# Kernel optimization log

Measured on AMD Instinct MI355X. Metric: run time of the kernel, lower is better.

The kernel has to match this reference:

```python
import jax, jax.numpy as jnp
import numpy as np

TEMP = 0.07
EPS = 1e-8
THRESH = 0.0          # self.global_threshold default
NORM_EPS = 1e-12      # F.normalize default eps


def setup_inputs() -> dict:
    key = jax.random.key(0)
    k1, k2, k3 = jax.random.split(key, 3)
    T, C, H, W = 8, 256, 64, 64
    return {
        "current_preds": jax.random.uniform(k1, (T, 1, H, W), jnp.float32),
        "history_preds": jax.random.uniform(k2, (T, 1, H, W), jnp.float32),
        "features": jax.random.normal(k3, (T, C, H, W), jnp.float32),
        "epoch": 1,
    }


def _supervised_labels(current_preds, history_preds):
    # Deviation per video (Dice-like metrics on binarized preds), then select
    # current pred if dev <= threshold else history pred (both detached).
    T = current_preds.shape[0]
    cb = (current_preds > 0.5).astype(jnp.float32).reshape(T, -1)
    hb = (history_preds > 0.5).astype(jnp.float32).reshape(T, -1)
    e1 = (cb * hb).sum(axis=1)
    e2 = cb.sum(axis=1) + hb.sum(axis=1)
    m1 = (2.0 * e1 + EPS) / (e2 + EPS)
    m2 = (e1 + EPS) / (e2 - e1 + EPS)
    dev = 1.0 - (m1 + m2) / 2.0                       # [T]
    use_curr = (dev <= THRESH)[:, None, None, None]
    return jnp.where(use_curr, current_preds, history_preds)


def _contrastive_loss(features, labels):
    T, C, H, W = features.shape
    N = H * W
    feat = features.reshape(T, C, N).transpose(0, 2, 1)            # [T,N,C]
    nrm = jnp.linalg.norm(feat, axis=-1, keepdims=True)
    feat = feat / jnp.maximum(nrm, NORM_EPS)                       # L2 normalize
    lbl = labels.reshape(T, N)
    fg = lbl > 0.5
    bg = ~fg
    sim = jnp.einsum('tnc,tmc->tnm', feat, feat) / TEMP            # [T,N,N]
    pos = jnp.exp(jnp.diagonal(sim, axis1=1, axis2=2))             # [T,N]
    # neg_i = sum over bg columns of exp(sim); masked matvec honors fg/bg split
    neg = jnp.einsum('tnm,tm->tn', jnp.exp(sim), bg.astype(feat.dtype))
    per_pix = -jnp.log(pos / (pos + neg + EPS))                    # [T,N]
    fgf = fg.astype(feat.dtype)
    n_fg = fgf.sum(axis=1)
    frame_loss = (per_pix * fgf).sum(axis=1) / jnp.maximum(n_fg, 1.0)  # mean over fg
    valid = (fg.any(axis=1) & bg.any(axis=1)).astype(feat.dtype)   # frames with both
    n_valid = valid.sum()
    return jnp.where(n_valid > 0,
                     (frame_loss * valid).sum() / jnp.maximum(n_valid, 1.0),
                     jnp.zeros((), feat.dtype))


def reference(current_preds, history_preds, features, epoch):
    # epoch >= 1 path of DOC.forward (epoch==0 only populates memory)
    labels = jax.lax.stop_gradient(_supervised_labels(current_preds, history_preds))
    loss = _contrastive_loss(features, labels)
    return (labels, loss)
```

## Files before the change

### kernel.cpp

```cpp
#include <hip/hip_runtime.h>
#include <hip/hip_bf16.h>
#include <cstdint>
#include <cstddef>

constexpr int T = 8;
constexpr int C = 256;
constexpr int N = 4096;
constexpr float TEMP_INV = 14.285714285714286f;
constexpr float EPS = 1e-8f;

typedef __bf16 bf16;
typedef __bf16 bf16x8 __attribute__((ext_vector_type(8)));
typedef float floatx4 __attribute__((ext_vector_type(4)));

__device__ __forceinline__ void async_copy16(const bf16* g, bf16* l) {
    __builtin_amdgcn_global_load_lds((const __attribute__((address_space(1))) void*)g,
                                     (__attribute__((address_space(3))) void*)l,
                                     16, 0, 0);
}

__global__ void stats_kernel(const float* __restrict__ cur,
                             const float* __restrict__ hist,
                             float* __restrict__ flag,
                             int* __restrict__ nfg, int* __restrict__ nbg) {
    int t = blockIdx.x;
    int tid = threadIdx.x;
    float s1 = 0.f, sc = 0.f, sh = 0.f;
    for (int k = tid; k < N; k += 256) {
        float c = cur[t * N + k] > 0.5f ? 1.f : 0.f;
        float h = hist[t * N + k] > 0.5f ? 1.f : 0.f;
        s1 += c * h; sc += c; sh += h;
    }
    for (int o = 32; o > 0; o >>= 1) {
        s1 += __shfl_down(s1, o);
        sc += __shfl_down(sc, o);
        sh += __shfl_down(sh, o);
    }
    __shared__ float r1[4], r2[4], r3[4];
    int w = tid >> 6;
    if ((tid & 63) == 0) { r1[w] = s1; r2[w] = sc; r3[w] = sh; }
    __syncthreads();
    if (tid == 0) {
        float e1 = r1[0] + r1[1] + r1[2] + r1[3];
        float scs = r2[0] + r2[1] + r2[2] + r2[3];
        float shs = r3[0] + r3[1] + r3[2] + r3[3];
        float e2 = scs + shs;
        float m1 = (2.f * e1 + EPS) / (e2 + EPS);
        float m2 = (e1 + EPS) / (e2 - e1 + EPS);
        float dev = 1.f - 0.5f * (m1 + m2);
        flag[t] = (dev <= 0.0f) ? 1.f : 0.f;
        nfg[t] = 0;
        nbg[t] = 0;
    }
}

__global__ void labels_kernel(const float* __restrict__ cur,
                              const float* __restrict__ hist,
                              const float* __restrict__ flag,
                              float* __restrict__ out_labels,
                              float* __restrict__ negbuf,
                              unsigned short* __restrict__ fgidx,
                              unsigned short* __restrict__ bgidx,
                              int* __restrict__ nfg, int* __restrict__ nbg) {
    int t = blockIdx.x;
    int tid = threadIdx.x;
    int lane = tid & 63;
    bool use_curr = flag[t] != 0.f;
    for (int it = 0; it < 4; ++it) {
        int p = it * 1024 + tid;
        int gi = t * N + p;
        float lab = use_curr ? cur[gi] : hist[gi];
        out_labels[gi] = lab;
        negbuf[gi] = 0.f;
        bool fg = lab > 0.5f;
        unsigned long long b = __ballot(fg);
        unsigned long long below = (lane == 0) ? 0ull : (b << (64 - lane)) >> (64 - lane);
        unsigned long long lowmask = (lane == 63) ? 0x7fffffffffffffffull
                                                  : ((1ull << lane) - 1ull);
        int rank_fg = __popcll(b & lowmask);
        int rank_bg = __popcll((~b) & lowmask);
        int cnt_fg = __popcll(b);
        int base_fg = 0, base_bg = 0;
        if (lane == 0) {
            base_fg = atomicAdd(&nfg[t], cnt_fg);
            base_bg = atomicAdd(&nbg[t], 64 - cnt_fg);
        }
        base_fg = __shfl(base_fg, 0);
        base_bg = __shfl(base_bg, 0);
        if (fg) fgidx[t * N + base_fg + rank_fg] = (unsigned short)p;
        else    bgidx[t * N + base_bg + rank_bg] = (unsigned short)p;
        (void)below;
    }
}

__global__ __launch_bounds__(256) void normalize_kernel(const float* __restrict__ feat,
                                                        bf16* __restrict__ fhat,
                                                        float* __restrict__ posdot) {
    __shared__ float tile[64 * 257];
    __shared__ float partial[256];
    __shared__ float rnorm_s[64];
    int t = blockIdx.x >> 6;
    int n0 = (blockIdx.x & 63) * 64;
    int tid = threadIdx.x;
    int lane63 = tid & 63;
    int w = tid >> 6;
    const float* fb = feat + (size_t)t * C * N;
    for (int it = 0; it < 64; ++it) {
        int c = w * 64 + it;
        tile[lane63 * 257 + c] = fb[(size_t)c * N + n0 + lane63];
    }
    __syncthreads();
    {
        int n = tid & 63, cp = tid >> 6;
        const float* row = &tile[n * 257 + cp * 64];
        float s = 0.f;
        for (int c = 0; c < 64; ++c) { float v = row[c]; s += v * v; }
        partial[tid] = s;
    }
    __syncthreads();
    if (tid < 64) {
        float s = partial[tid] + partial[tid + 64] + partial[tid + 128] + partial[tid + 192];
        float nrm = sqrtf(s);
        float r = 1.f / fmaxf(nrm, 1e-12f);
        rnorm_s[tid] = r;
        posdot[t * N + n0 + tid] = s * r * r;
    }
    __syncthreads();
    bf16* ob = fhat + ((size_t)t * N + n0) * C;
    for (int it = 0; it < 8; ++it) {
        int l = it * 256 + tid;
        int n = l >> 5;
        int c = (l & 31) * 8;
        float r = rnorm_s[n];
        const float* src = &tile[n * 257 + c];
        bf16x8 v;
        for (int j = 0; j < 8; ++j) v[j] = (bf16)(src[j] * r);
        *(bf16x8*)(ob + l * 8) = v;
    }
}

__global__ __launch_bounds__(256, 2) void sim_kernel(const bf16* __restrict__ fhat,
                                                     const unsigned short* __restrict__ fgidx,
                                                     const unsigned short* __restrict__ bgidx,
                                                     const int* __restrict__ nfg,
                                                     const int* __restrict__ nbg,
                                                     float* __restrict__ neg) {
    int t = blockIdx.z;
    int nfgt = nfg[t];
    int nbgt = nbg[t];
    int rowbase = blockIdx.y * 128;
    int colbase = blockIdx.x * 128;
    if (rowbase >= nfgt || colbase >= nbgt) return;

    __shared__ bf16 a_lds[128 * 64];
    __shared__ bf16 b_lds[128 * 64];
    int tid = threadIdx.x;
    int lane = tid & 63;
    int w = tid >> 6;
    const bf16* fb = fhat + (size_t)t * N * C;

    int ch = (lane & 7) ^ (lane >> 3);
    int r0w = (w & 1) * 64;
    int c0w = (w >> 1) * 64;

    const bf16* arp[4];
    const bf16* brp[4];
    for (int s = 0; s < 4; ++s) {
        int q = w * 4 + s;
        int row_l = q * 8 + (lane >> 3);
        int ra = rowbase + row_l; if (ra >= nfgt) ra = nfgt - 1;
        int rb = colbase + row_l; if (rb >= nbgt) rb = nbgt - 1;
        arp[s] = fb + (size_t)fgidx[t * N + ra] * C + ch * 8;
        brp[s] = fb + (size_t)bgidx[t * N + rb] * C + ch * 8;
    }

    floatx4 acc[4][4];
    for (int i = 0; i < 4; ++i)
        for (int j = 0; j < 4; ++j)
            acc[i][j] = (floatx4){0.f, 0.f, 0.f, 0.f};

    for (int ks = 0; ks < 4; ++ks) {
        int k0 = ks * 64;
        __syncthreads();
        for (int s = 0; s < 4; ++s) {
            int q = w * 4 + s;
            async_copy16(arp[s] + k0, &a_lds[q * 512]);
            async_copy16(brp[s] + k0, &b_lds[q * 512]);
        }
        __syncthreads();
        for (int kk = 0; kk < 64; kk += 32) {
            int quad = lane >> 4;
            int chread = (kk >> 3) + quad;
            bf16x8 af[4], bfr[4];
            for (int i = 0; i < 4; ++i) {
                int r = r0w + 16 * i + (lane & 15);
                int chs = chread ^ (r & 7);
                af[i] = *(const bf16x8*)&a_lds[r * 64 + chs * 8];
            }
            for (int j = 0; j < 4; ++j) {
                int cidx = c0w + 16 * j + (lane & 15);
                int chs = chread ^ (cidx & 7);
                bfr[j] = *(const bf16x8*)&b_lds[cidx * 64 + chs * 8];
            }
            for (int i = 0; i < 4; ++i)
                for (int j = 0; j < 4; ++j)
                    acc[i][j] = __builtin_amdgcn_mfma_f32_16x16x32_bf16(af[i], bfr[j], acc[i][j], 0, 0, 0);
        }
    }

    float bgv[4];
    for (int j = 0; j < 4; ++j) {
        int cidx = colbase + c0w + 16 * j + (lane & 15);
        bgv[j] = (cidx < nbgt) ? 1.f : 0.f;
    }

    int quad = lane >> 4;
    for (int i = 0; i < 4; ++i) {
        for (int reg = 0; reg < 4; ++reg) {
            float msum = 0.f;
            for (int j = 0; j < 4; ++j)
                msum += __expf(acc[i][j][reg] * TEMP_INV) * bgv[j];
            msum += __shfl_xor(msum, 1);
            msum += __shfl_xor(msum, 2);
            msum += __shfl_xor(msum, 4);
            msum += __shfl_xor(msum, 8);
            if ((lane & 15) == 0) {
                int row = rowbase + r0w + 16 * i + quad * 4 + reg;
                if (row < nfgt) atomicAdd(&neg[t * N + row], msum);
            }
        }
    }
}

__global__ void loss_frame_kernel(const float* __restrict__ negbuf,
                                  const float* __restrict__ posdot,
                                  const unsigned short* __restrict__ fgidx,
                                  const int* __restrict__ nfg,
                                  const int* __restrict__ nbg,
                                  float* __restrict__ framebuf) {
    int t = blockIdx.x;
    int tid = threadIdx.x;
    int nfgt = nfg[t];
    float s = 0.f;
    for (int k = tid; k < nfgt; k += 256) {
        int pix = fgidx[t * N + k];
        float pos = __expf(posdot[t * N + pix] * TEMP_INV);
        float ng = negbuf[t * N + k];
        s += logf((pos + ng + EPS) / pos);
    }
    for (int o = 32; o > 0; o >>= 1) s += __shfl_down(s, o);
    __shared__ float r[4];
    if ((tid & 63) == 0) r[tid >> 6] = s;
    __syncthreads();
    if (tid == 0) {
        float tot = r[0] + r[1] + r[2] + r[3];
        float fl = tot / fmaxf((float)nfgt, 1.f);
        float valid = (nfgt > 0 && nbg[t] > 0) ? 1.f : 0.f;
        framebuf[t] = fl * valid;
        framebuf[8 + t] = valid;
    }
}

__global__ void loss_final_kernel(const float* __restrict__ framebuf,
                                  float* __restrict__ out_loss) {
    if (threadIdx.x == 0) {
        float s = 0.f, v = 0.f;
        for (int t = 0; t < T; ++t) { s += framebuf[t]; v += framebuf[8 + t]; }
        out_loss[0] = (v > 0.f) ? s / fmaxf(v, 1.f) : 0.f;
    }
}

extern "C" void kernel_launch(void* const* d_in, const int* in_sizes, int n_in,
                              void* d_out, int out_size, void* d_ws, size_t ws_size,
                              hipStream_t stream) {
    const float* cur  = (const float*)d_in[0];
    const float* hist = (const float*)d_in[1];
    const float* feat = (const float*)d_in[2];
    float* out = (float*)d_out;

    char* ws = (char*)d_ws;
    bf16*  fhat    = (bf16*)ws;
    float* negbuf  = (float*)(ws + 16777216);
    float* posdot  = (float*)(ws + 16908288);
    unsigned short* fgidx = (unsigned short*)(ws + 17039360);
    unsigned short* bgidx = (unsigned short*)(ws + 17104896);
    float* flag    = (float*)(ws + 17170432);
    int*   nfg     = (int*)(ws + 17170432 + 64);
    int*   nbg     = nfg + 8;
    float* framebuf = (float*)(nbg + 8);

    stats_kernel<<<8, 256, 0, stream>>>(cur, hist, flag, nfg, nbg);
    labels_kernel<<<8, 1024, 0, stream>>>(cur, hist, flag, out, negbuf, fgidx, bgidx, nfg, nbg);
    normalize_kernel<<<512, 256, 0, stream>>>(feat, fhat, posdot);
    dim3 g(32, 32, 8);
    sim_kernel<<<g, 256, 0, stream>>>(fhat, fgidx, bgidx, nfg, nbg, negbuf);
    loss_frame_kernel<<<8, 256, 0, stream>>>(negbuf, posdot, fgidx, nfg, nbg, framebuf);
    loss_final_kernel<<<1, 64, 0, stream>>>(framebuf, out + 32768);
}
```

Measured before the change: 170.6 us.

## Persistent double-buffered sim kernel, bf16 normalize tile, fused loss kernels

The sim kernel becomes persistent: 512 blocks stride over the (frame, row-tile, col-tile) space. It double-buffers the LDS K-slices so the async global-to-LDS copy of the next slice overlaps the MFMA work on the current one. Normalize computes the sum of squares during the load and stores the tile as bf16, which shrinks LDS use and drops one sync. The labels kernel is split across 64 smaller blocks, and the two loss kernels are merged into one launch. The risks are double rounding in normalize (bf16 before scaling) and extra LDS in sim that may lower occupancy.

```diff
diff --git a/kernel.cpp b/kernel.cpp
--- a/kernel.cpp
+++ b/kernel.cpp
@@ -62,19 +62,19 @@
                               unsigned short* __restrict__ fgidx,
                               unsigned short* __restrict__ bgidx,
                               int* __restrict__ nfg, int* __restrict__ nbg) {
-    int t = blockIdx.x;
+    int t = blockIdx.x >> 3;
+    int seg = (blockIdx.x & 7) * 512;
     int tid = threadIdx.x;
     int lane = tid & 63;
     bool use_curr = flag[t] != 0.f;
-    for (int it = 0; it < 4; ++it) {
-        int p = it * 1024 + tid;
+    for (int it = 0; it < 2; ++it) {
+        int p = seg + it * 256 + tid;
         int gi = t * N + p;
         float lab = use_curr ? cur[gi] : hist[gi];
         out_labels[gi] = lab;
         negbuf[gi] = 0.f;
         bool fg = lab > 0.5f;
         unsigned long long b = __ballot(fg);
-        unsigned long long below = (lane == 0) ? 0ull : (b << (64 - lane)) >> (64 - lane);
         unsigned long long lowmask = (lane == 63) ? 0x7fffffffffffffffull
                                                   : ((1ull << lane) - 1ull);
         int rank_fg = __popcll(b & lowmask);
@@ -89,14 +89,13 @@
         base_bg = __shfl(base_bg, 0);
         if (fg) fgidx[t * N + base_fg + rank_fg] = (unsigned short)p;
         else    bgidx[t * N + base_bg + rank_bg] = (unsigned short)p;
-        (void)below;
     }
 }
 
 __global__ __launch_bounds__(256) void normalize_kernel(const float* __restrict__ feat,
                                                         bf16* __restrict__ fhat,
                                                         float* __restrict__ posdot) {
-    __shared__ float tile[64 * 257];
+    __shared__ bf16 tile[64 * 258];
     __shared__ float partial[256];
     __shared__ float rnorm_s[64];
     int t = blockIdx.x >> 6;
@@ -105,23 +104,18 @@
     int lane63 = tid & 63;
     int w = tid >> 6;
     const float* fb = feat + (size_t)t * C * N;
+    float ss = 0.f;
     for (int it = 0; it < 64; ++it) {
         int c = w * 64 + it;
-        tile[lane63 * 257 + c] = fb[(size_t)c * N + n0 + lane63];
-    }
-    __syncthreads();
-    {
-        int n = tid & 63, cp = tid >> 6;
-        const float* row = &tile[n * 257 + cp * 64];
-        float s = 0.f;
-        for (int c = 0; c < 64; ++c) { float v = row[c]; s += v * v; }
-        partial[tid] = s;
-    }
+        float v = fb[(size_t)c * N + n0 + lane63];
+        ss += v * v;
+        tile[lane63 * 258 + c] = (bf16)v;
+    }
+    partial[tid] = ss;
     __syncthreads();
     if (tid < 64) {
         float s = partial[tid] + partial[tid + 64] + partial[tid + 128] + partial[tid + 192];
-        float nrm = sqrtf(s);
-        float r = 1.f / fmaxf(nrm, 1e-12f);
+        float r = 1.f / fmaxf(sqrtf(s), 1e-12f);
         rnorm_s[tid] = r;
         posdot[t * N + n0 + tid] = s * r * r;
     }
@@ -132,10 +126,10 @@
         int n = l >> 5;
         int c = (l & 31) * 8;
         float r = rnorm_s[n];
-        const float* src = &tile[n * 257 + c];
-        bf16x8 v;
-        for (int j = 0; j < 8; ++j) v[j] = (bf16)(src[j] * r);
-        *(bf16x8*)(ob + l * 8) = v;
+        bf16x8 vin = *(const bf16x8*)&tile[n * 258 + c];
+        bf16x8 vo;
+        for (int j = 0; j < 8; ++j) vo[j] = (bf16)((float)vin[j] * r);
+        *(bf16x8*)(ob + l * 8) = vo;
     }
 }
 
@@ -145,128 +139,131 @@
                                                      const int* __restrict__ nfg,
                                                      const int* __restrict__ nbg,
                                                      float* __restrict__ neg) {
-    int t = blockIdx.z;
-    int nfgt = nfg[t];
-    int nbgt = nbg[t];
-    int rowbase = blockIdx.y * 128;
-    int colbase = blockIdx.x * 128;
-    if (rowbase >= nfgt || colbase >= nbgt) return;
-
-    __shared__ bf16 a_lds[128 * 64];
-    __shared__ bf16 b_lds[128 * 64];
+    __shared__ bf16 a_lds[2][128 * 64];
+    __shared__ bf16 b_lds[2][128 * 64];
     int tid = threadIdx.x;
     int lane = tid & 63;
     int w = tid >> 6;
-    const bf16* fb = fhat + (size_t)t * N * C;
-
     int ch = (lane & 7) ^ (lane >> 3);
     int r0w = (w & 1) * 64;
     int c0w = (w >> 1) * 64;
-
-    const bf16* arp[4];
-    const bf16* brp[4];
-    for (int s = 0; s < 4; ++s) {
-        int q = w * 4 + s;
-        int row_l = q * 8 + (lane >> 3);
-        int ra = rowbase + row_l; if (ra >= nfgt) ra = nfgt - 1;
-        int rb = colbase + row_l; if (rb >= nbgt) rb = nbgt - 1;
-        arp[s] = fb + (size_t)fgidx[t * N + ra] * C + ch * 8;
-        brp[s] = fb + (size_t)bgidx[t * N + rb] * C + ch * 8;
-    }
-
-    floatx4 acc[4][4];
-    for (int i = 0; i < 4; ++i)
-        for (int j = 0; j < 4; ++j)
-            acc[i][j] = (floatx4){0.f, 0.f, 0.f, 0.f};
-
-    for (int ks = 0; ks < 4; ++ks) {
-        int k0 = ks * 64;
-        __syncthreads();
+    int quad = lane >> 4;
+
+    for (int vt = blockIdx.x; vt < T * 32 * 32; vt += 512) {
+        int t = vt >> 10;
+        int rem = vt & 1023;
+        int rowbase = (rem >> 5) * 128;
+        int colbase = (rem & 31) * 128;
+        int nfgt = nfg[t];
+        int nbgt = nbg[t];
+        if (rowbase >= nfgt || colbase >= nbgt) continue;
+
+        const bf16* fb = fhat + (size_t)t * N * C;
+        const bf16* arp[4];
+        const bf16* brp[4];
         for (int s = 0; s < 4; ++s) {
             int q = w * 4 + s;
-            async_copy16(arp[s] + k0, &a_lds[q * 512]);
-            async_copy16(brp[s] + k0, &b_lds[q * 512]);
-        }
-        __syncthreads();
-        for (int kk = 0; kk < 64; kk += 32) {
-            int quad = lane >> 4;
-            int chread = (kk >> 3) + quad;
-            bf16x8 af[4], bfr[4];
-            for (int i = 0; i < 4; ++i) {
-                int r = r0w + 16 * i + (lane & 15);
-                int chs = chread ^ (r & 7);
-                af[i] = *(const bf16x8*)&a_lds[r * 64 + chs * 8];
+            int row_l = q * 8 + (lane >> 3);
+            int ra = rowbase + row_l; if (ra >= nfgt) ra = nfgt - 1;
+            int rb = colbase + row_l; if (rb >= nbgt) rb = nbgt - 1;
+            arp[s] = fb + (size_t)fgidx[t * N + ra] * C + ch * 8;
+            brp[s] = fb + (size_t)bgidx[t * N + rb] * C + ch * 8;
+        }
+
+        floatx4 acc[4][4];
+        for (int i = 0; i < 4; ++i)
+            for (int j = 0; j < 4; ++j)
+                acc[i][j] = (floatx4){0.f, 0.f, 0.f, 0.f};
+
+        for (int s = 0; s < 4; ++s) {
+            int q = w * 4 + s;
+            async_copy16(arp[s], &a_lds[0][q * 512]);
+            async_copy16(brp[s], &b_lds[0][q * 512]);
+        }
+
+        for (int ks = 0; ks < 4; ++ks) {
+            int buf = ks & 1;
+            __syncthreads();
+            if (ks < 3) {
+                int k0 = (ks + 1) * 64;
+                int nb2 = buf ^ 1;
+                for (int s = 0; s < 4; ++s) {
+                    int q = w * 4 + s;
+                    async_copy16(arp[s] + k0, &a_lds[nb2][q * 512]);
+                    async_copy16(brp[s] + k0, &b_lds[nb2][q * 512]);
+                }
             }
-            for (int j = 0; j < 4; ++j) {
-                int cidx = c0w + 16 * j + (lane & 15);
-                int chs = chread ^ (cidx & 7);
-                bfr[j] = *(const bf16x8*)&b_lds[cidx * 64 + chs * 8];
+            for (int kk = 0; kk < 64; kk += 32) {
+                int chread = (kk >> 3) + quad;
+                bf16x8 af[4], bfr[4];
+                for (int i = 0; i < 4; ++i) {
+                    int r = r0w + 16 * i + (lane & 15);
+                    int chs = chread ^ (r & 7);
+                    af[i] = *(const bf16x8*)&a_lds[buf][r * 64 + chs * 8];
+                }
+                for (int j = 0; j < 4; ++j) {
+                    int cidx = c0w + 16 * j + (lane & 15);
+                    int chs = chread ^ (cidx & 7);
+                    bfr[j] = *(const bf16x8*)&b_lds[buf][cidx * 64 + chs * 8];
+                }
+                for (int i = 0; i < 4; ++i)
+                    for (int j = 0; j < 4; ++j)
+                        acc[i][j] = __builtin_amdgcn_mfma_f32_16x16x32_bf16(af[i], bfr[j], acc[i][j], 0, 0, 0);
             }
-            for (int i = 0; i < 4; ++i)
+        }
+
+        float bgv[4];
+        for (int j = 0; j < 4; ++j) {
+            int cidx = colbase + c0w + 16 * j + (lane & 15);
+            bgv[j] = (cidx < nbgt) ? 1.f : 0.f;
+        }
+        for (int i = 0; i < 4; ++i) {
+            for (int reg = 0; reg < 4; ++reg) {
+                float msum = 0.f;
                 for (int j = 0; j < 4; ++j)
-                    acc[i][j] = __builtin_amdgcn_mfma_f32_16x16x32_bf16(af[i], bfr[j], acc[i][j], 0, 0, 0);
-        }
-    }
-
-    float bgv[4];
-    for (int j = 0; j < 4; ++j) {
-        int cidx = colbase + c0w + 16 * j + (lane & 15);
-        bgv[j] = (cidx < nbgt) ? 1.f : 0.f;
-    }
-
-    int quad = lane >> 4;
-    for (int i = 0; i < 4; ++i) {
-        for (int reg = 0; reg < 4; ++reg) {
-            float msum = 0.f;
-            for (int j = 0; j < 4; ++j)
-                msum += __expf(acc[i][j][reg] * TEMP_INV) * bgv[j];
-            msum += __shfl_xor(msum, 1);
-            msum += __shfl_xor(msum, 2);
-            msum += __shfl_xor(msum, 4);
-            msum += __shfl_xor(msum, 8);
-            if ((lane & 15) == 0) {
-                int row = rowbase + r0w + 16 * i + quad * 4 + reg;
-                if (row < nfgt) atomicAdd(&neg[t * N + row], msum);
+                    msum += __expf(acc[i][j][reg] * TEMP_INV) * bgv[j];
+                msum += __shfl_xor(msum, 1);
+                msum += __shfl_xor(msum, 2);
+                msum += __shfl_xor(msum, 4);
+                msum += __shfl_xor(msum, 8);
+                if ((lane & 15) == 0) {
+                    int row = rowbase + r0w + 16 * i + quad * 4 + reg;
+                    if (row < nfgt) atomicAdd(&neg[t * N + row], msum);
+                }
             }
         }
     }
 }
 
-__global__ void loss_frame_kernel(const float* __restrict__ negbuf,
-                                  const float* __restrict__ posdot,
-                                  const unsigned short* __restrict__ fgidx,
-                                  const int* __restrict__ nfg,
-                                  const int* __restrict__ nbg,
-                                  float* __restrict__ framebuf) {
-    int t = blockIdx.x;
-    int tid = threadIdx.x;
+__global__ void loss_kernel(const float* __restrict__ negbuf,
+                            const float* __restrict__ posdot,
+                            const unsigned short* __restrict__ fgidx,
+                            const int* __restrict__ nfg,
+                            const int* __restrict__ nbg,
+                            float* __restrict__ out_loss) {
+    int tid = threadIdx.x;
+    int t = tid >> 6;
+    int lane = tid & 63;
     int nfgt = nfg[t];
     float s = 0.f;
-    for (int k = tid; k < nfgt; k += 256) {
+    for (int k = lane; k < nfgt; k += 64) {
         int pix = fgidx[t * N + k];
         float pos = __expf(posdot[t * N + pix] * TEMP_INV);
         float ng = negbuf[t * N + k];
         s += logf((pos + ng + EPS) / pos);
     }
     for (int o = 32; o > 0; o >>= 1) s += __shfl_down(s, o);
-    __shared__ float r[4];
-    if ((tid & 63) == 0) r[tid >> 6] = s;
+    __shared__ float fl[8], vv[8];
+    if (lane == 0) {
+        float valid = (nfgt > 0 && nbg[t] > 0) ? 1.f : 0.f;
+        fl[t] = valid * (s / fmaxf((float)nfgt, 1.f));
+        vv[t] = valid;
+    }
     __syncthreads();
     if (tid == 0) {
-        float tot = r[0] + r[1] + r[2] + r[3];
-        float fl = tot / fmaxf((float)nfgt, 1.f);
-        float valid = (nfgt > 0 && nbg[t] > 0) ? 1.f : 0.f;
-        framebuf[t] = fl * valid;
-        framebuf[8 + t] = valid;
-    }
-}
-
-__global__ void loss_final_kernel(const float* __restrict__ framebuf,
-                                  float* __restrict__ out_loss) {
-    if (threadIdx.x == 0) {
-        float s = 0.f, v = 0.f;
-        for (int t = 0; t < T; ++t) { s += framebuf[t]; v += framebuf[8 + t]; }
-        out_loss[0] = (v > 0.f) ? s / fmaxf(v, 1.f) : 0.f;
+        float ls = 0.f, v = 0.f;
+        for (int i = 0; i < T; ++i) { ls += fl[i]; v += vv[i]; }
+        out_loss[0] = (v > 0.f) ? ls / fmaxf(v, 1.f) : 0.f;
     }
 }
 
@@ -287,13 +284,10 @@
     float* flag    = (float*)(ws + 17170432);
     int*   nfg     = (int*)(ws + 17170432 + 64);
     int*   nbg     = nfg + 8;
-    float* framebuf = (float*)(nbg + 8);
 
     stats_kernel<<<8, 256, 0, stream>>>(cur, hist, flag, nfg, nbg);
-    labels_kernel<<<8, 1024, 0, stream>>>(cur, hist, flag, out, negbuf, fgidx, bgidx, nfg, nbg);
+    labels_kernel<<<64, 256, 0, stream>>>(cur, hist, flag, out, negbuf, fgidx, bgidx, nfg, nbg);
     normalize_kernel<<<512, 256, 0, stream>>>(feat, fhat, posdot);
-    dim3 g(32, 32, 8);
-    sim_kernel<<<g, 256, 0, stream>>>(fhat, fgidx, bgidx, nfg, nbg, negbuf);
-    loss_frame_kernel<<<8, 256, 0, stream>>>(negbuf, posdot, fgidx, nfg, nbg, framebuf);
-    loss_final_kernel<<<1, 64, 0, stream>>>(framebuf, out + 32768);
-}
+    sim_kernel<<<512, 256, 0, stream>>>(fhat, fgidx, bgidx, nfg, nbg, negbuf);
+    loss_kernel<<<1, 512, 0, stream>>>(negbuf, posdot, fgidx, nfg, nbg, out + 32768);
+}
```

Result: slower. 230.8 us (+35.3%).
